# Kernel optimization log

Measured on AMD Instinct MI355X. Metric: run time of the kernel, lower is better.

Reference implementation:

```python
import jax, jax.numpy as jnp
import numpy as np

B = 64
NUM_ENT = 40000
NUM_REL = 1345
DIM = 200
N_LIT = 100


def setup_inputs() -> dict:
    key = jax.random.key(0)
    ks = jax.random.split(key, 8)
    e1_idx = jax.random.randint(ks[0], (B,), 0, NUM_ENT)
    r_idx = jax.random.randint(ks[1], (B,), 0, NUM_REL)
    E_weight = jax.random.normal(ks[2], (NUM_ENT, DIM), dtype=jnp.float32) * 0.1
    R_weight = jax.random.normal(ks[3], (NUM_REL, DIM), dtype=jnp.float32) * 0.1
    # numerical literals are min-max normalized to [0, 1]
    num_lit = jax.random.uniform(ks[4], (NUM_ENT, N_LIT), dtype=jnp.float32)
    c = jax.random.normal(ks[5], (N_LIT,), dtype=jnp.float32) * 0.1
    var = jax.random.uniform(ks[6], (N_LIT,), dtype=jnp.float32) * 0.1 + 1e-3  # positive
    nf_weights = jax.random.normal(ks[7], (NUM_REL, N_LIT), dtype=jnp.float32) * 0.1
    return {"e1_idx": e1_idx, "r_idx": r_idx, "E_weight": E_weight,
            "R_weight": R_weight, "num_lit": num_lit, "c": c, "var": var,
            "nf_weights": nf_weights}


def reference(e1_idx, r_idx, E_weight, R_weight, num_lit, c, var, nf_weights):
    # Dropout is identity in eval mode.
    e1 = E_weight[e1_idx]                      # [B, D]
    r = R_weight[r_idx]                        # [B, D]
    score_l = jnp.einsum('bd,ed->be', e1 * r, E_weight)   # [B, E]

    n_h = num_lit[e1_idx]                      # [B, L]
    # broadcast instead of repeat: [B, 1, L] - [1, E, L] -> [B, E, L]
    n = n_h[:, None, :] - num_lit[None, :, :]
    phi = jnp.exp(-((n - c) ** 2) / var)       # RBF, [B, E, L]
    w_nf = nf_weights[r_idx]                   # [B, L]
    score_n = jnp.einsum('bel,bl->be', phi, w_nf)          # [B, E]

    return jax.nn.sigmoid(score_l + score_n)
```

## Files before the change

### kernel.cpp

```cpp
#include <hip/hip_runtime.h>

#define NB 64
#define NE 40000
#define DIM 200
#define NL 100
#define EBLK 32
#define NTHREADS 256
#define D4 50
#define L4 25
#define LOG2E 1.4426950408889634f

#define WS_E1R 0
#define WS_ASW 28672

#define A_OFF    0
#define BM_OFF   16384
#define SCAT_OFF 0
#define XS_OFF   0
#define SMEM_BYTES 24576

typedef float f32x4 __attribute__((ext_vector_type(4)));
typedef short bf16x8 __attribute__((ext_vector_type(8)));

__device__ __forceinline__ unsigned int f2bf(float f) {
    unsigned int u = __float_as_uint(f);
    return (u + 0x7fffu + ((u >> 16) & 1u)) >> 16;
}
__device__ __forceinline__ unsigned int packbf(float a, float b) {
    return f2bf(a) | (f2bf(b) << 16);
}

__global__ void DistMult_prep_kernel(
    const int* __restrict__ e1_idx, const int* __restrict__ r_idx,
    const float* __restrict__ Ew, const float* __restrict__ Rw,
    const float* __restrict__ num_lit, const float* __restrict__ cvec,
    const float* __restrict__ var, const float* __restrict__ nfw,
    unsigned char* __restrict__ ws)
{
    const int t = blockIdx.x * NTHREADS + threadIdx.x;
    unsigned int* e1r = (unsigned int*)(ws + WS_E1R);
    const float4* E4 = (const float4*)Ew;
    const float4* R4 = (const float4*)Rw;

    for (int f = t; f < NB * 28; f += 8 * NTHREADS) {
        int b = f / 28, c = f % 28;
        uint4 st = {0u, 0u, 0u, 0u};
        if (c < 25) {
            float4 a0 = E4[(size_t)e1_idx[b] * D4 + 2 * c];
            float4 a1 = E4[(size_t)e1_idx[b] * D4 + 2 * c + 1];
            float4 r0 = R4[(size_t)r_idx[b] * D4 + 2 * c];
            float4 r1 = R4[(size_t)r_idx[b] * D4 + 2 * c + 1];
            st.x = packbf(a0.x * r0.x, a0.y * r0.y);
            st.y = packbf(a0.z * r0.z, a0.w * r0.w);
            st.z = packbf(a1.x * r1.x, a1.y * r1.y);
            st.w = packbf(a1.z * r1.z, a1.w * r1.w);
        }
        *(uint4*)(e1r + (size_t)b * 112 + c * 4) = st;
    }

    float2* asw = (float2*)(ws + WS_ASW);
    for (int f = t; f < NL * NB; f += 8 * NTHREADS) {
        int b = f & 63, l = f >> 6;
        float s = sqrtf(LOG2E / var[l]);
        float2 v;
        v.x = (num_lit[(size_t)e1_idx[b] * NL + l] - cvec[l]) * s;
        v.y = nfw[(size_t)r_idx[b] * NL + l];
        asw[f] = v;
    }
}

__global__ __launch_bounds__(NTHREADS, 6)
void DistMult_KBLN_79164837200204_kernel(
    const float* __restrict__ Ew, const float* __restrict__ num_lit,
    const float* __restrict__ var,
    const unsigned char* __restrict__ ws, float* __restrict__ out)
{
    __shared__ __align__(16) char smem[SMEM_BYTES];
    __shared__ float sS[NL];

    const int t = threadIdx.x;
    const int nq = (NE / EBLK) >> 3, nr = (NE / EBLK) & 7;
    const int xcd = blockIdx.x & 7, sub = blockIdx.x >> 3;
    const int wg = (xcd < nr ? xcd * (nq + 1) : nr * (nq + 1) + (xcd - nr) * nq) + sub;
    const int e0 = wg * EBLK;

    const int L = t & 63, w = t >> 6;
    const int l15 = L & 15, lq = L >> 4;
    const int tx = t & 7, ty = t >> 3;

    if (t < NL) sS[t] = sqrtf(LOG2E / var[t]);

    unsigned short* pA  = (unsigned short*)(smem + A_OFF);
    unsigned short* pBm = (unsigned short*)(smem + BM_OFF);
    for (int i = t; i < 1024; i += NTHREADS) ((unsigned int*)pA)[i] = 0u;
    for (int i = t; i < 512;  i += NTHREADS) ((unsigned int*)pBm)[i] = 0u;
    __syncthreads();
    if (t < 64) {
        pA[t * 32]     = (unsigned short)f2bf(256.0f * t);
        pA[t * 32 + 1] = (unsigned short)f2bf(1.0f);
    } else if (t < 96) {
        int e = t - 64;
        pBm[e * 32]     = (unsigned short)f2bf(1.0f);
        pBm[e * 32 + 1] = (unsigned short)f2bf((float)e);
    }
    __syncthreads();
    int ib0[4], ib1[4];
    {
        bf16x8 afp = *(const bf16x8*)(pA + (16 * w + l15) * 32 + lq * 8);
        bf16x8 b0p = *(const bf16x8*)(pBm + l15 * 32 + lq * 8);
        bf16x8 b1p = *(const bf16x8*)(pBm + (16 + l15) * 32 + lq * 8);
        f32x4 z = {0.f, 0.f, 0.f, 0.f};
        f32x4 p0 = __builtin_amdgcn_mfma_f32_16x16x32_bf16(afp, b0p, z, 0, 0, 0);
        f32x4 p1 = __builtin_amdgcn_mfma_f32_16x16x32_bf16(afp, b1p, z, 0, 0, 0);
        #pragma unroll
        for (int r = 0; r < 4; ++r) { ib0[r] = (int)p0[r]; ib1[r] = (int)p1[r]; }
    }
    __syncthreads();

    f32x4 acc0 = {0.f, 0.f, 0.f, 0.f};
    f32x4 acc1 = {0.f, 0.f, 0.f, 0.f};

    const float4* E4 = (const float4*)Ew;
    const uint4* wsA = (const uint4*)(ws + WS_E1R);

    #pragma unroll
    for (int h = 0; h < 2; ++h) {
        const int nc = h ? 12 : 16;
        for (int f = t; f < NB * nc; f += NTHREADS) {
            int b = f / nc, c = f % nc;
            uint4 v = wsA[(size_t)b * 28 + h * 16 + c];
            int off = (b * 256 + c * 16) ^ ((b & 7) << 4);
            *(uint4*)(smem + A_OFF + off) = v;
        }
        for (int f = t; f < EBLK * nc; f += NTHREADS) {
            int e = f / nc, c = f % nc;
            int dg = h * 128 + c * 8;
            uint4 st = {0u, 0u, 0u, 0u};
            if (dg <= DIM - 8) {
                float4 v0 = E4[(size_t)(e0 + e) * D4 + (dg >> 2)];
                float4 v1 = E4[(size_t)(e0 + e) * D4 + (dg >> 2) + 1];
                st.x = packbf(v0.x, v0.y);
                st.y = packbf(v0.z, v0.w);
                st.z = packbf(v1.x, v1.y);
                st.w = packbf(v1.z, v1.w);
            }
            int off = (e * 256 + c * 16) ^ ((e & 7) << 4);
            *(uint4*)(smem + BM_OFF + off) = st;
        }
        __syncthreads();

        const int nst = h ? 3 : 4;
        const int arow = 16 * w + l15;
        const int aswz = (arow & 7) << 4;
        const int bswz = (l15 & 7) << 4;
        #pragma unroll
        for (int s = 0; s < 4; ++s) {
            if (s < nst) {
                int kb = s * 64 + lq * 16;
                bf16x8 af = *(const bf16x8*)(smem + A_OFF + ((arow * 256 + kb) ^ aswz));
                bf16x8 b0 = *(const bf16x8*)(smem + BM_OFF + ((l15 * 256 + kb) ^ bswz));
                bf16x8 b1 = *(const bf16x8*)(smem + BM_OFF + (((16 + l15) * 256 + kb) ^ bswz));
                acc0 = __builtin_amdgcn_mfma_f32_16x16x32_bf16(af, b0, acc0, 0, 0, 0);
                acc1 = __builtin_amdgcn_mfma_f32_16x16x32_bf16(af, b1, acc1, 0, 0, 0);
            }
        }
        __syncthreads();
    }

    float* scat = (float*)(smem + SCAT_OFF);
    #pragma unroll
    for (int r = 0; r < 4; ++r) {
        scat[(ib0[r] >> 8) * 33 + (ib0[r] & 255)] = acc0[r];
        scat[(ib1[r] >> 8) * 33 + (ib1[r] & 255)] = acc1[r];
    }
    __syncthreads();

    float2 acc2[4];
    #pragma unroll
    for (int j = 0; j < 4; ++j) {
        acc2[j].x = scat[(2 * ty) * 33 + 4 * tx + j];
        acc2[j].y = scat[(2 * ty + 1) * 33 + 4 * tx + j];
    }
    __syncthreads();

    const float4* N4 = (const float4*)num_lit;
    float* xsF = (float*)(smem + XS_OFF);
    for (int f = t; f < EBLK * L4; f += NTHREADS) {
        int e = f & 31, l4 = f >> 5;
        float4 v = N4[(size_t)(e0 + e) * L4 + l4];
        const float* vf = (const float*)&v;
        #pragma unroll
        for (int k = 0; k < 4; ++k)
            xsF[(4 * l4 + k) * 32 + e] = vf[k] * sS[4 * l4 + k];
    }
    __syncthreads();

    const float4* ASW = (const float4*)(ws + WS_ASW);
    #pragma unroll 4
    for (int l = 0; l < NL; ++l) {
        float4 aw = ASW[l * 32 + ty];
        float4 xs = *(const float4*)(xsF + l * 32 + 4 * tx);
        float xj[4] = { xs.x, xs.y, xs.z, xs.w };
        #pragma unroll
        for (int j = 0; j < 4; ++j) {
            float m0 = aw.x - xj[j];
            float m1 = aw.z - xj[j];
            float p0 = __builtin_amdgcn_exp2f(-(m0 * m0));
            float p1 = __builtin_amdgcn_exp2f(-(m1 * m1));
            acc2[j].x = fmaf(p0, aw.y, acc2[j].x);
            acc2[j].y = fmaf(p1, aw.w, acc2[j].y);
        }
    }

    {
        float4 o0, o1;
        float* p0 = (float*)&o0;
        float* p1 = (float*)&o1;
        #pragma unroll
        for (int j = 0; j < 4; ++j) {
            float ex0 = __builtin_amdgcn_exp2f(-LOG2E * acc2[j].x);
            float ex1 = __builtin_amdgcn_exp2f(-LOG2E * acc2[j].y);
            p0[j] = __builtin_amdgcn_rcpf(1.0f + ex0);
            p1[j] = __builtin_amdgcn_rcpf(1.0f + ex1);
        }
        size_t b0 = 2 * ty;
        *(float4*)&out[b0 * NE + e0 + 4 * tx] = o0;
        *(float4*)&out[(b0 + 1) * NE + e0 + 4 * tx] = o1;
    }
}

extern "C" void kernel_launch(void* const* d_in, const int* in_sizes, int n_in,
                              void* d_out, int out_size, void* d_ws, size_t ws_size,
                              hipStream_t stream) {
    const int*   e1_idx  = (const int*)d_in[0];
    const int*   r_idx   = (const int*)d_in[1];
    const float* Ew      = (const float*)d_in[2];
    const float* Rw      = (const float*)d_in[3];
    const float* num_lit = (const float*)d_in[4];
    const float* cvec    = (const float*)d_in[5];
    const float* var     = (const float*)d_in[6];
    const float* nfw     = (const float*)d_in[7];
    float* out = (float*)d_out;

    DistMult_prep_kernel<<<8, NTHREADS, 0, stream>>>(
        e1_idx, r_idx, Ew, Rw, num_lit, cvec, var, nfw, (unsigned char*)d_ws);
    DistMult_KBLN_79164837200204_kernel<<<NE / EBLK, NTHREADS, 0, stream>>>(
        Ew, num_lit, var, (const unsigned char*)d_ws, out);
}
```

Before: 55.22 us.

## Halve entity tile, read A operand from global, shrink LDS for occupancy

Entity block size drops from 32 to 16, so the grid doubles and each wave issues one MFMA per step instead of two. The bf16 e1*r A operand is now read straight from the global workspace rather than staged in LDS, and LDS drops to 8KB with launch bounds raised to 8 blocks per SM. The RBF workspace changes to a b-major layout so each thread reads two literals per float4. This trades LDS staging and per-block reuse for higher occupancy and parallelism, at the cost of more global/L2 traffic for the A operand and duplicated setup work across twice as many blocks.

```diff
diff --git a/kernel.cpp b/kernel.cpp
--- a/kernel.cpp
+++ b/kernel.cpp
@@ -4,7 +4,7 @@
 #define NE 40000
 #define DIM 200
 #define NL 100
-#define EBLK 32
+#define EBLK 16
 #define NTHREADS 256
 #define D4 50
 #define L4 25
@@ -13,11 +13,12 @@
 #define WS_E1R 0
 #define WS_ASW 28672
 
-#define A_OFF    0
-#define BM_OFF   16384
+#define PA_OFF   0
+#define PB_OFF   4096
+#define BM_OFF   0
 #define SCAT_OFF 0
 #define XS_OFF   0
-#define SMEM_BYTES 24576
+#define SMEM_BYTES 8192
 
 typedef float f32x4 __attribute__((ext_vector_type(4)));
 typedef short bf16x8 __attribute__((ext_vector_type(8)));
@@ -60,7 +61,7 @@
 
     float2* asw = (float2*)(ws + WS_ASW);
     for (int f = t; f < NL * NB; f += 8 * NTHREADS) {
-        int b = f & 63, l = f >> 6;
+        int b = f / NL, l = f - b * NL;
         float s = sqrtf(LOG2E / var[l]);
         float2 v;
         v.x = (num_lit[(size_t)e1_idx[b] * NL + l] - cvec[l]) * s;
@@ -69,7 +70,7 @@
     }
 }
 
-__global__ __launch_bounds__(NTHREADS, 6)
+__global__ __launch_bounds__(NTHREADS, 8)
 void DistMult_KBLN_79164837200204_kernel(
     const float* __restrict__ Ew, const float* __restrict__ num_lit,
     const float* __restrict__ var,
@@ -86,52 +87,41 @@
 
     const int L = t & 63, w = t >> 6;
     const int l15 = L & 15, lq = L >> 4;
-    const int tx = t & 7, ty = t >> 3;
+    const int tx = t & 3, ty = t >> 2;
 
     if (t < NL) sS[t] = sqrtf(LOG2E / var[t]);
 
-    unsigned short* pA  = (unsigned short*)(smem + A_OFF);
-    unsigned short* pBm = (unsigned short*)(smem + BM_OFF);
+    unsigned short* pA = (unsigned short*)(smem + PA_OFF);
+    unsigned short* pB = (unsigned short*)(smem + PB_OFF);
     for (int i = t; i < 1024; i += NTHREADS) ((unsigned int*)pA)[i] = 0u;
-    for (int i = t; i < 512;  i += NTHREADS) ((unsigned int*)pBm)[i] = 0u;
+    for (int i = t; i < 256;  i += NTHREADS) ((unsigned int*)pB)[i] = 0u;
     __syncthreads();
     if (t < 64) {
         pA[t * 32]     = (unsigned short)f2bf(256.0f * t);
         pA[t * 32 + 1] = (unsigned short)f2bf(1.0f);
-    } else if (t < 96) {
+    } else if (t < 80) {
         int e = t - 64;
-        pBm[e * 32]     = (unsigned short)f2bf(1.0f);
-        pBm[e * 32 + 1] = (unsigned short)f2bf((float)e);
-    }
-    __syncthreads();
-    int ib0[4], ib1[4];
+        pB[e * 32]     = (unsigned short)f2bf(1.0f);
+        pB[e * 32 + 1] = (unsigned short)f2bf((float)e);
+    }
+    __syncthreads();
+    int ib0[4];
     {
         bf16x8 afp = *(const bf16x8*)(pA + (16 * w + l15) * 32 + lq * 8);
-        bf16x8 b0p = *(const bf16x8*)(pBm + l15 * 32 + lq * 8);
-        bf16x8 b1p = *(const bf16x8*)(pBm + (16 + l15) * 32 + lq * 8);
+        bf16x8 b0p = *(const bf16x8*)(pB + l15 * 32 + lq * 8);
         f32x4 z = {0.f, 0.f, 0.f, 0.f};
         f32x4 p0 = __builtin_amdgcn_mfma_f32_16x16x32_bf16(afp, b0p, z, 0, 0, 0);
-        f32x4 p1 = __builtin_amdgcn_mfma_f32_16x16x32_bf16(afp, b1p, z, 0, 0, 0);
-        #pragma unroll
-        for (int r = 0; r < 4; ++r) { ib0[r] = (int)p0[r]; ib1[r] = (int)p1[r]; }
+        #pragma unroll
+        for (int r = 0; r < 4; ++r) ib0[r] = (int)p0[r];
     }
     __syncthreads();
 
     f32x4 acc0 = {0.f, 0.f, 0.f, 0.f};
-    f32x4 acc1 = {0.f, 0.f, 0.f, 0.f};
-
     const float4* E4 = (const float4*)Ew;
-    const uint4* wsA = (const uint4*)(ws + WS_E1R);
 
     #pragma unroll
     for (int h = 0; h < 2; ++h) {
         const int nc = h ? 12 : 16;
-        for (int f = t; f < NB * nc; f += NTHREADS) {
-            int b = f / nc, c = f % nc;
-            uint4 v = wsA[(size_t)b * 28 + h * 16 + c];
-            int off = (b * 256 + c * 16) ^ ((b & 7) << 4);
-            *(uint4*)(smem + A_OFF + off) = v;
-        }
         for (int f = t; f < EBLK * nc; f += NTHREADS) {
             int e = f / nc, c = f % nc;
             int dg = h * 128 + c * 8;
@@ -151,17 +141,14 @@
 
         const int nst = h ? 3 : 4;
         const int arow = 16 * w + l15;
-        const int aswz = (arow & 7) << 4;
         const int bswz = (l15 & 7) << 4;
         #pragma unroll
         for (int s = 0; s < 4; ++s) {
             if (s < nst) {
                 int kb = s * 64 + lq * 16;
-                bf16x8 af = *(const bf16x8*)(smem + A_OFF + ((arow * 256 + kb) ^ aswz));
+                bf16x8 af = *(const bf16x8*)(ws + WS_E1R + arow * 448 + h * 256 + kb);
                 bf16x8 b0 = *(const bf16x8*)(smem + BM_OFF + ((l15 * 256 + kb) ^ bswz));
-                bf16x8 b1 = *(const bf16x8*)(smem + BM_OFF + (((16 + l15) * 256 + kb) ^ bswz));
                 acc0 = __builtin_amdgcn_mfma_f32_16x16x32_bf16(af, b0, acc0, 0, 0, 0);
-                acc1 = __builtin_amdgcn_mfma_f32_16x16x32_bf16(af, b1, acc1, 0, 0, 0);
             }
         }
         __syncthreads();
@@ -169,63 +156,59 @@
 
     float* scat = (float*)(smem + SCAT_OFF);
     #pragma unroll
-    for (int r = 0; r < 4; ++r) {
-        scat[(ib0[r] >> 8) * 33 + (ib0[r] & 255)] = acc0[r];
-        scat[(ib1[r] >> 8) * 33 + (ib1[r] & 255)] = acc1[r];
-    }
-    __syncthreads();
-
-    float2 acc2[4];
+    for (int r = 0; r < 4; ++r)
+        scat[(ib0[r] >> 8) * 17 + (ib0[r] & 255)] = acc0[r];
+    __syncthreads();
+
+    float acc[4];
     #pragma unroll
-    for (int j = 0; j < 4; ++j) {
-        acc2[j].x = scat[(2 * ty) * 33 + 4 * tx + j];
-        acc2[j].y = scat[(2 * ty + 1) * 33 + 4 * tx + j];
-    }
+    for (int j = 0; j < 4; ++j)
+        acc[j] = scat[ty * 17 + 4 * tx + j];
     __syncthreads();
 
     const float4* N4 = (const float4*)num_lit;
     float* xsF = (float*)(smem + XS_OFF);
     for (int f = t; f < EBLK * L4; f += NTHREADS) {
-        int e = f & 31, l4 = f >> 5;
+        int e = f & 15, l4 = f >> 4;
         float4 v = N4[(size_t)(e0 + e) * L4 + l4];
         const float* vf = (const float*)&v;
         #pragma unroll
         for (int k = 0; k < 4; ++k)
-            xsF[(4 * l4 + k) * 32 + e] = vf[k] * sS[4 * l4 + k];
-    }
-    __syncthreads();
-
-    const float4* ASW = (const float4*)(ws + WS_ASW);
-    #pragma unroll 4
-    for (int l = 0; l < NL; ++l) {
-        float4 aw = ASW[l * 32 + ty];
-        float4 xs = *(const float4*)(xsF + l * 32 + 4 * tx);
-        float xj[4] = { xs.x, xs.y, xs.z, xs.w };
+            xsF[(4 * l4 + k) * 20 + e] = vf[k] * sS[4 * l4 + k];
+    }
+    __syncthreads();
+
+    const float4* ASWB = (const float4*)(ws + WS_ASW);
+    #pragma unroll 2
+    for (int l2 = 0; l2 < NL / 2; ++l2) {
+        float4 awp = ASWB[ty * 50 + l2];
+        float4 xa = *(const float4*)(xsF + (2 * l2) * 20 + 4 * tx);
+        float4 xb = *(const float4*)(xsF + (2 * l2 + 1) * 20 + 4 * tx);
+        float xja[4] = { xa.x, xa.y, xa.z, xa.w };
+        float xjb[4] = { xb.x, xb.y, xb.z, xb.w };
         #pragma unroll
         for (int j = 0; j < 4; ++j) {
-            float m0 = aw.x - xj[j];
-            float m1 = aw.z - xj[j];
+            float m0 = awp.x - xja[j];
             float p0 = __builtin_amdgcn_exp2f(-(m0 * m0));
+            acc[j] = fmaf(p0, awp.y, acc[j]);
+        }
+        #pragma unroll
+        for (int j = 0; j < 4; ++j) {
+            float m1 = awp.z - xjb[j];
             float p1 = __builtin_amdgcn_exp2f(-(m1 * m1));
-            acc2[j].x = fmaf(p0, aw.y, acc2[j].x);
-            acc2[j].y = fmaf(p1, aw.w, acc2[j].y);
+            acc[j] = fmaf(p1, awp.w, acc[j]);
         }
     }
 
     {
-        float4 o0, o1;
-        float* p0 = (float*)&o0;
-        float* p1 = (float*)&o1;
+        float4 o;
+        float* op = (float*)&o;
         #pragma unroll
         for (int j = 0; j < 4; ++j) {
-            float ex0 = __builtin_amdgcn_exp2f(-LOG2E * acc2[j].x);
-            float ex1 = __builtin_amdgcn_exp2f(-LOG2E * acc2[j].y);
-            p0[j] = __builtin_amdgcn_rcpf(1.0f + ex0);
-            p1[j] = __builtin_amdgcn_rcpf(1.0f + ex1);
-        }
-        size_t b0 = 2 * ty;
-        *(float4*)&out[b0 * NE + e0 + 4 * tx] = o0;
-        *(float4*)&out[(b0 + 1) * NE + e0 + 4 * tx] = o1;
+            float ex = __builtin_amdgcn_exp2f(-LOG2E * acc[j]);
+            op[j] = __builtin_amdgcn_rcpf(1.0f + ex);
+        }
+        *(float4*)&out[(size_t)ty * NE + e0 + 4 * tx] = o;
     }
 }
 
```

Measured after the change: 53.89 us. 2.4% less time.
